# Performance work log

Measured on AMD Instinct MI355X. Metric: run time of the kernel, lower is better.

## Reference

```python
import jax, jax.numpy as jnp
import numpy as np
import math

N0, E, D_IN, H, NC, UH = 4096, 65536, 128, 256, 10, 64
K1 = math.ceil(0.8 * N0)   # 3277 nodes kept by pool1
K2 = math.ceil(0.2 * K1)   # 656 nodes kept by pool2

PARAM_SHAPES = dict(
    gcn1_w=(D_IN, H), gcn1_b=(H,), pool1_w=(H,), gcn2_w=(H, H), gcn2_b=(H,), pool2_w=(H,),
    inr_w=(H, H), inr_b=(H,), ini_w=(H, H), ini_b=(H,),
    enc1_w=(1, UH), enc1_b=(UH,), enc2_w=(UH, UH), enc2_b=(UH,),
    p1_w=(UH, UH), p1_b=(UH,), p2_w=(UH, UH // 2), p2_b=(UH // 2,),
    p3_w=(UH // 2, K2 * K2), p3_b=(K2 * K2,),
    rt_w=(H, H), rt_b=(H,), it_w=(H, H), it_b=(H,),
    msg_wr=(H, H), msg_wi=(H, H),
    mc1_w=(H, H // 2), mc1_b=(H // 2,), mc2_w=(H // 2, NC), mc2_b=(NC,),
    pc1_w=(H, H // 2), pc1_b=(H // 2,), pc2_w=(H // 2, NC), pc2_b=(NC,),
)

def gcn_conv(x, src, dst, emask, W, b):
    # GCNConv: self-loops + symmetric normalization; emask zeroes edges dropped by pooling
    n = x.shape[0]
    h = x @ W
    deg = jnp.zeros((n,), h.dtype).at[dst].add(emask) + 1.0
    dis = jax.lax.rsqrt(deg)
    coef = dis[src] * dis[dst] * emask
    out = jnp.zeros_like(h).at[dst].add(coef[:, None] * h[src])
    out = out + (dis * dis)[:, None] * h   # self-loop contribution
    return out + b

def topk_pool(x, src, dst, emask, w, k):
    # PyG TopKPooling: score = x@w/||w||, keep top-k, x <- x[perm]*tanh(score[perm])
    n = x.shape[0]
    score = (x @ w) / jnp.linalg.norm(w)
    _, perm = jax.lax.top_k(score, k)
    x_new = x[perm] * jnp.tanh(score[perm])[:, None]
    mapping = jnp.full((n,), -1, jnp.int32).at[perm].set(jnp.arange(k, dtype=jnp.int32))
    ns, nd = mapping[src], mapping[dst]
    nm = emask * (ns >= 0) * (nd >= 0)
    return x_new, jnp.maximum(ns, 0), jnp.maximum(nd, 0), nm

def herm_sqrt(C):
    C = (C + C.conj().T) * 0.5
    w, V = jnp.linalg.eigh(C)
    w = jnp.maximum(w, 0.0)
    return (V * jnp.sqrt(w + 1e-8)) @ V.conj().T

def forward(x, edge_index, P):
    src, dst = edge_index[0], edge_index[1]
    em = jnp.ones((src.shape[0],), jnp.float32)
    h = jax.nn.relu(gcn_conv(x, src, dst, em, P['gcn1_w'], P['gcn1_b']))
    h, src, dst, em = topk_pool(h, src, dst, em, P['pool1_w'], K1)
    h = jax.nn.relu(gcn_conv(h, src, dst, em, P['gcn2_w'], P['gcn2_b']))
    h, src, dst, em = topk_pool(h, src, dst, em, P['pool2_w'], K2)
    xr = h @ P['inr_w'] + P['inr_b']
    xi = h @ P['ini_w'] + P['ini_b']
    # --- LocalQuantumLayer (eval mode: dropout is identity) ---
    # ImprovedUnitaryDilationNetwork on the pooled graph (N = K2)
    xg = jnp.ones((K2, 1), jnp.float32)
    xg = jax.nn.relu(gcn_conv(xg, src, dst, em, P['enc1_w'], P['enc1_b']))
    xg = gcn_conv(xg, src, dst, em, P['enc2_w'], P['enc2_b'])
    emb = xg.mean(0)                                     # global_mean_pool, single graph
    t = jax.nn.relu(emb @ P['p1_w'] + P['p1_b'])
    t = jax.nn.relu(t @ P['p2_w'] + P['p2_b'])
    pm = jnp.tanh(t @ P['p3_w'] + P['p3_b']).reshape(K2, K2)
    A = 0.05 * ((pm - pm.T) * 0.5 + 1j * (pm + pm.T) * 0.5)  # antihermitian, scaled
    U = jax.scipy.linalg.expm(A)
    I = jnp.eye(K2, dtype=U.dtype)
    S1 = jax.lax.stop_gradient(herm_sqrt(I - U.conj().T @ U))
    S2 = jax.lax.stop_gradient(herm_sqrt(I - U @ U.conj().T))
    U_dil = jnp.concatenate([jnp.concatenate([U, S1], 1),
                             jnp.concatenate([S2, -U.conj().T], 1)], 0)
    xrt = jax.nn.relu(xr @ P['rt_w'] + P['rt_b'])
    xit = jax.nn.relu(xi @ P['it_w'] + P['it_b'])
    xc = xrt + 1j * xit
    # unitary_dim = 2*K2 > K2 nodes -> single batch, U_sub = U_dil[:K2,:K2]
    evolved = U_dil[:K2, :K2] @ xc
    Wm = P['msg_wr'] + 1j * P['msg_wi']
    msg = evolved[src] @ Wm                              # message(x_j) = x_j @ W (complex)
    agg = jnp.zeros_like(xc).at[dst].add(msg * em[:, None])  # aggr='add'
    outc = agg + (xr + 1j * xi)                          # identity residual (dims equal)
    mag = jnp.abs(outc)
    ph = jnp.arctan2(outc.imag, outc.real)
    gm, gp = mag.mean(0), ph.mean(0)                     # global_mean_pool, single graph
    lm = jax.nn.relu(gm @ P['mc1_w'] + P['mc1_b']) @ P['mc2_w'] + P['mc2_b']
    lp = jax.nn.relu(gp @ P['pc1_w'] + P['pc1_b']) @ P['pc2_w'] + P['pc2_b']
    return lm + lp

def setup_inputs() -> dict:
    key = jax.random.key(0)
    ks = iter(jax.random.split(key, 64))
    inp = {}
    inp['x'] = jax.random.normal(next(ks), (N0, D_IN), jnp.float32)
    inp['edge_index'] = jax.random.randint(next(ks), (2, E), 0, N0)
    for name, shp in PARAM_SHAPES.items():
        inp[name] = jax.random.normal(next(ks), shp, jnp.float32) * 0.05
    return inp

def reference(x, edge_index, gcn1_w, gcn1_b, pool1_w, gcn2_w, gcn2_b, pool2_w, inr_w, inr_b, ini_w, ini_b, enc1_w, enc1_b, enc2_w, enc2_b, p1_w, p1_b, p2_w, p2_b, p3_w, p3_b, rt_w, rt_b, it_w, it_b, msg_wr, msg_wi, mc1_w, mc1_b, mc2_w, mc2_b, pc1_w, pc1_b, pc2_w, pc2_b):
    P = dict(locals())
    x_ = P.pop('x'); ei = P.pop('edge_index')
    return forward(x_, ei, P)
```

## Files before the change

### kernel.cpp

```cpp
#include <hip/hip_runtime.h>
#include <cstddef>
#include <utility>

constexpr int N0  = 4096;
constexpr int E   = 65536;
constexpr int DIN = 128;
constexpr int HD  = 256;
constexpr int NC  = 10;
constexpr int UHD = 64;
constexpr int K1  = 3277;
constexpr int K2  = 656;
constexpr int PMN = K2 * K2;

constexpr int SQ_SLOTS = 4;

constexpr int PLD = 704;
constexpr size_t PPS = (size_t)PLD * PLD;

constexpr int CSPLIT = 8;

#define F4(n) ((size_t)(n) * 4)
constexpr size_t O_H1    = 0;
constexpr size_t O_OUT1  = O_H1    + F4(N0 * HD);
constexpr size_t O_DEG1  = O_OUT1  + F4(N0 * HD);
constexpr size_t O_DIS1  = O_DEG1  + F4(N0);
constexpr size_t O_SC1   = O_DIS1  + F4(N0);
constexpr size_t O_PERM1 = O_SC1   + F4(N0);
constexpr size_t O_MAP1  = O_PERM1 + F4(N0);
constexpr size_t O_H1P   = O_MAP1  + F4(N0);
constexpr size_t O_SRC2  = O_H1P   + F4(K1 * HD);
constexpr size_t O_DST2  = O_SRC2  + F4(E);
constexpr size_t O_EM2   = O_DST2  + F4(E);
constexpr size_t O_H2    = O_EM2   + F4(E);
constexpr size_t O_OUT2  = O_H2    + F4(K1 * HD);
constexpr size_t O_DEG2  = O_OUT2  + F4(K1 * HD);
constexpr size_t O_DIS2  = O_DEG2  + F4(N0);
constexpr size_t O_SC2   = O_DIS2  + F4(N0);
constexpr size_t O_PERM2 = O_SC2   + F4(N0);
constexpr size_t O_MAP2  = O_PERM2 + F4(N0);
constexpr size_t O_H2P   = O_MAP2  + F4(N0);
constexpr size_t O_SRC3  = O_H2P   + F4(K2 * HD);
constexpr size_t O_DST3  = O_SRC3  + F4(E);
constexpr size_t O_EM3   = O_DST3  + F4(E);
constexpr size_t O_XR    = O_EM3   + F4(E);
constexpr size_t O_XI    = O_XR    + F4(K2 * HD);
constexpr size_t O_DEG3  = O_XI    + F4(K2 * HD);
constexpr size_t O_DIS3  = O_DEG3  + F4(1024);
constexpr size_t O_SCOEF = O_DIS3  + F4(1024);
constexpr size_t O_XG1   = O_SCOEF + F4(1024);
constexpr size_t O_XG2H  = O_XG1   + F4(K2 * UHD);
constexpr size_t O_XG2   = O_XG2H  + F4(K2 * UHD);
constexpr size_t O_EMB   = O_XG2   + F4(K2 * UHD);
constexpr size_t O_T1    = O_EMB   + F4(64);
constexpr size_t O_T2    = O_T1    + F4(64);
constexpr size_t O_NORM  = O_T2    + F4(64);
constexpr size_t O_PM    = O_NORM  + F4(64);
constexpr size_t O_BM    = O_PM    + F4(PMN);
constexpr size_t O_P0    = O_BM    + F4(PMN) * 2;
constexpr size_t O_P1    = O_P0    + F4(PMN) * 2;
constexpr size_t O_XRT   = O_P1    + F4(PMN) * 2;
constexpr size_t O_XIT   = O_XRT   + F4(K2 * HD);
constexpr size_t O_XC    = O_XIT   + F4(K2 * HD);
constexpr size_t O_EVO   = O_XC    + F4(K2 * HD) * 2;
constexpr size_t O_AGG0  = O_EVO   + F4(K2 * HD) * 2;
constexpr size_t O_WC    = O_AGG0  + F4(K2 * HD) * 2;
constexpr size_t O_AGG1  = O_WC    + F4(HD * HD) * 2;
constexpr size_t O_MAG   = O_AGG1  + F4(K2 * HD) * 2;
constexpr size_t O_PH    = O_MAG   + F4(K2 * HD);
constexpr size_t O_GM    = O_PH    + F4(K2 * HD);
constexpr size_t O_GP    = O_GM    + F4(256);
constexpr size_t O_HM    = O_GP    + F4(256);
constexpr size_t O_HP    = O_HM    + F4(256);
constexpr size_t O_LM    = O_HP    + F4(256);
constexpr size_t O_LP    = O_LM    + F4(64);
constexpr size_t WS_NEED = O_LP    + F4(64);

constexpr size_t O_SA = 0;
constexpr size_t O_ST = O_SA + PPS * 2 * 4;
static_assert(O_ST + PPS * 2 * 4 <= O_SRC3, "SA/ST must fit in dead region");

constexpr size_t O_B2 = O_XRT;
static_assert(O_B2 + F4(PMN) * 2 <= O_MAG, "B2 must fit in XRT..AGG1 region");

constexpr size_t O_CSR_OFF = O_MAG;
constexpr size_t O_CSR_CUR = O_CSR_OFF + F4(4104);
constexpr size_t O_CSR_SRC = O_CSR_CUR + F4(4104);
constexpr size_t O_CSR_CF  = O_CSR_SRC + F4(E);
static_assert(O_CSR_CF + F4(E) <= O_GM, "CSR must fit in MAG/PH region");

constexpr size_t O_PARTX  = (WS_NEED + 255) & ~(size_t)255;
constexpr size_t PART_SZ  = (size_t)CSPLIT * PMN * 8;
constexpr size_t WS_TOTAL = O_PARTX + PART_SZ;

typedef __attribute__((ext_vector_type(8))) short s8v;
typedef __attribute__((ext_vector_type(4))) float f4v;

__device__ inline unsigned short f2bf(float x) {
  unsigned u = __float_as_uint(x);
  u += 0x7FFFu + ((u >> 16) & 1u);
  return (unsigned short)(u >> 16);
}
__device__ inline float bf2f(unsigned short h) {
  return __uint_as_float(((unsigned)h) << 16);
}
__device__ inline void split4(float re, float im, unsigned short* out,
                              size_t ps, size_t o) {
  unsigned short rh = f2bf(re);
  unsigned short rl = f2bf(re - bf2f(rh));
  unsigned short ih = f2bf(im);
  unsigned short il = f2bf(im - bf2f(ih));
  out[o] = rh; out[ps + o] = rl; out[2 * ps + o] = ih; out[3 * ps + o] = il;
}


template <int ACT>
__global__ void rmm64(const float* __restrict__ A, const float* __restrict__ B,
                      const float* __restrict__ bias, float* __restrict__ C,
                      int M, int N, int K, int CS, int CO) {
  __shared__ float As[64][17];
  __shared__ float Bs[16][64];
  int t  = threadIdx.x;
  int tx = t & 15, ty = t >> 4;
  int bm = blockIdx.y * 64, bn = blockIdx.x * 64;
  float ra[4], rb[4];
#pragma unroll
  for (int i = 0; i < 4; i++) {
    int l = t + i * 256;
    int gr = bm + (l >> 4);
    ra[i] = (gr < M) ? A[(size_t)gr * K + (l & 15)] : 0.f;
    int gc = bn + (l & 63);
    rb[i] = (gc < N) ? B[(size_t)(l >> 6) * N + gc] : 0.f;
  }
  float acc[4][4] = {};
  for (int kt = 0; kt < K; kt += 16) {
#pragma unroll
    for (int i = 0; i < 4; i++) {
      int l = t + i * 256;
      As[l >> 4][l & 15] = ra[i];
      Bs[l >> 6][l & 63] = rb[i];
    }
    __syncthreads();
    int kn = kt + 16;
    if (kn < K) {
#pragma unroll
      for (int i = 0; i < 4; i++) {
// ... 95 lines not shown
  for (int i = 0; i < 4; i++) {
    int r = bm + ty + 16 * i;
    if (r >= M) continue;
#pragma unroll
    for (int j = 0; j < 4; j++) {
      int c = bn + tx + 16 * j;
      if (c >= N) continue;
      float v = acc[i][j] + (bias ? bias[c] : 0.f);
      if (ACT == 1) v = fmaxf(v, 0.f);
      C[((size_t)r * N + c) * CS] = v;
    }
  }
}

__global__ void split_planesT(const float2* __restrict__ in, int inM, int inN,
                              unsigned short* __restrict__ out, int padR, int ld,
                              size_t ps) {
  __shared__ float2 tile[32][33];
  int tx = threadIdx.x & 31, ty = threadIdx.x >> 5;
  int k0 = blockIdx.x * 32, n0 = blockIdx.y * 32;
  for (int i = ty; i < 32; i += 8) {
    int k = k0 + i, n = n0 + tx;
    tile[i][tx] = (k < inM && n < inN) ? in[(size_t)k * inN + n]
                                       : make_float2(0.f, 0.f);
  }
  __syncthreads();
  for (int i = ty; i < 32; i += 8) {
    int n = n0 + i, k = k0 + tx;
    if (n < padR && k < ld)
      split4(tile[tx][i].x, tile[tx][i].y, out, ps, (size_t)n * ld + k);
  }
}

__global__ void split_planesT2(const float* __restrict__ re, const float* __restrict__ im,
                               int inM, int inN, unsigned short* __restrict__ out,
                               int padR, int ld, size_t ps) {
  __shared__ float2 tile[32][33];
  int tx = threadIdx.x & 31, ty = threadIdx.x >> 5;
  int k0 = blockIdx.x * 32, n0 = blockIdx.y * 32;
  for (int i = ty; i < 32; i += 8) {
    int k = k0 + i, n = n0 + tx;
    tile[i][tx] = (k < inM && n < inN)
        ? make_float2(re[(size_t)k * inN + n], im[(size_t)k * inN + n])
        : make_float2(0.f, 0.f);
  }
  __syncthreads();
  for (int i = ty; i < 32; i += 8) {
    int n = n0 + i, k = k0 + tx;
    if (n < padR && k < ld)
      split4(tile[tx][i].x, tile[tx][i].y, out, ps, (size_t)n * ld + k);
  }
}

__global__ __launch_bounds__(256, 2) void cmm_bf16_sk(
    const unsigned short* __restrict__ SA, size_t psA, int ldA,
    const unsigned short* __restrict__ ST, size_t psT, int ldT,
    float2* __restrict__ Part, int M, int N, int Kp, int chunk,
    const int* __restrict__ gate, int slot) {
  if (gate && slot >= *gate - 1) return;
  __shared__ unsigned short Bl[2][4 * 64 * 32];
  int k0 = blockIdx.x * chunk;
  int kend = min(Kp, k0 + chunk);
  int t = threadIdx.x;
  int wave = t >> 6, lane = t & 63;
  int quad = lane >> 4, mn = lane & 15;
  int rowA = blockIdx.z * 64 + wave * 16 + mn;
  int bn = blockIdx.y * 64;
  const unsigned short* a0 = SA + (size_t)rowA * ldA;
  int pB = t >> 6, cB_ = t & 63;
  const unsigned short* bsrc = ST + (size_t)(bn + cB_) * ldT + pB * psT;
  f4v accR[4], accI[4];
#pragma unroll
  for (int i = 0; i < 4; i++) {
    accR[i] = (f4v){0.f, 0.f, 0.f, 0.f};
    accI[i] = (f4v){0.f, 0.f, 0.f, 0.f};
  }
  s8v cA[4], nA[4], rB[4], nB[4];
  {
    int ka = k0 + quad * 8;
#pragma unroll
    for (int p = 0; p < 4; p++) cA[p] = *(const s8v*)(a0 + p * psA + ka);
#pragma unroll
    for (int j = 0; j < 4; j++) rB[j] = *(const s8v*)(bsrc + k0 + j * 8);
  }
  int it = 0;
  for (int kt = k0; kt < kend; kt += 32, ++it) {
    int buf = it & 1;
    unsigned short* bl = &Bl[buf][(size_t)t * 32];
#pragma unroll
    for (int j = 0; j < 4; j++) *(s8v*)(bl + j * 8) = rB[j];
    __syncthreads();
    int kn = kt + 32;
    if (kn < kend) {
      int ka = kn + quad * 8;
#pragma unroll
      for (int p = 0; p < 4; p++) nA[p] = *(const s8v*)(a0 + p * psA + ka);
#pragma unroll
      for (int j = 0; j < 4; j++) nB[j] = *(const s8v*)(bsrc + kn + j * 8);
    }
    s8v nih, nil_;
#pragma unroll
    for (int q = 0; q < 8; q++) {
      nih[q]  = (short)(cA[2][q] ^ (short)0x8000);
      nil_[q] = (short)(cA[3][q] ^ (short)0x8000);
    }
#pragma unroll
    for (int tl = 0; tl < 4; tl++) {
      int c = tl * 16 + mn;
      s8v b0 = *(const s8v*)&Bl[buf][(0 * 64 + c) * 32 + quad * 8];
      s8v b1 = *(const s8v*)&Bl[buf][(1 * 64 + c) * 32 + quad * 8];
      s8v b2 = *(const s8v*)&Bl[buf][(2 * 64 + c) * 32 + quad * 8];
      s8v b3 = *(const s8v*)&Bl[buf][(3 * 64 + c) * 32 + quad * 8];
      f4v r = accR[tl];
      r = __builtin_amdgcn_mfma_f32_16x16x32_bf16(cA[0], b0, r, 0, 0, 0);
      r = __builtin_amdgcn_mfma_f32_16x16x32_bf16(cA[1], b0, r, 0, 0, 0);
      r = __builtin_amdgcn_mfma_f32_16x16x32_bf16(cA[0], b1, r, 0, 0, 0);
      r = __builtin_amdgcn_mfma_f32_16x16x32_bf16(nih, b2, r, 0, 0, 0);
      r = __builtin_amdgcn_mfma_f32_16x16x32_bf16(nil_, b2, r, 0, 0, 0);
      r = __builtin_amdgcn_mfma_f32_16x16x32_bf16(nih, b3, r, 0, 0, 0);
      accR[tl] = r;
      f4v im = accI[tl];
      im = __builtin_amdgcn_mfma_f32_16x16x32_bf16(cA[0], b2, im, 0, 0, 0);
      im = __builtin_amdgcn_mfma_f32_16x16x32_bf16(cA[1], b2, im, 0, 0, 0);
      im = __builtin_amdgcn_mfma_f32_16x16x32_bf16(cA[0], b3, im, 0, 0, 0);
      im = __builtin_amdgcn_mfma_f32_16x16x32_bf16(cA[2], b0, im, 0, 0, 0);
      im = __builtin_amdgcn_mfma_f32_16x16x32_bf16(cA[3], b0, im, 0, 0, 0);
      im = __builtin_amdgcn_mfma_f32_16x16x32_bf16(cA[2], b1, im, 0, 0, 0);
      accI[tl] = im;
    }
    if (kn < kend) {
#pragma unroll
      for (int p = 0; p < 4; p++) cA[p] = nA[p];
#pragma unroll
      for (int j = 0; j < 4; j++) rB[j] = nB[j];
    }
  }
  float2* P = Part + (size_t)blockIdx.x * M * N;
#pragma unroll
  for (int tl = 0; tl < 4; tl++) {
    int col = bn + tl * 16 + mn;
    if (col >= N) continue;
#pragma unroll
    for (int r = 0; r < 4; r++) {
      int row = blockIdx.z * 64 + wave * 16 + quad * 4 + r;
      if (row >= M) continue;
      P[(size_t)row * N + col] = make_float2(accR[tl][r], accI[tl][r]);
    }
  }
}

__global__ void creduce(const float2* __restrict__ Part, float2* __restrict__ C,
                        int MN, int N, int S, float e0,
                        const float2* __restrict__ E1, float e1,
                        const float2* __restrict__ E2, float e2) {
  int idx = blockIdx.x * 256 + threadIdx.x;
  if (idx >= MN) return;
  float sr = 0.f, si = 0.f;
  for (int z = 0; z < S; z++) {
    float2 p = Part[(size_t)z * MN + idx];
    sr += p.x;
    si += p.y;
  }
  if (e0 != 0.f) {
    int r = idx / N;
    if (idx - r * N == r) sr += e0;
  }
  if (E1) { float2 b = E1[idx]; sr += e1 * b.x; si += e1 * b.y; }
  if (E2) { float2 b = E2[idx]; sr += e2 * b.x; si += e2 * b.y; }
  C[idx] = make_float2(sr, si);
}

template <int WC_, int WSA, int WST>
__global__ void creduce_tiled(const float2* __restrict__ Part, int S, int M, int N,
                              int RP, int CP, float2* __restrict__ C,
                              unsigned short* __restrict__ SAp, size_t psA,
                              unsigned short* __restrict__ STp, size_t psT,
                              float e0, const float2* __restrict__ E1, float e1,
                              const float2* __restrict__ E2, float e2,
                              const int* __restrict__ gate, int slot) {
  if (gate && slot >= *gate - 1) return;
  __shared__ float vr[32][33], vi[32][33];
  int tx = threadIdx.x & 31, ty = threadIdx.x >> 5;
  int r0 = blockIdx.y * 32, c0 = blockIdx.x * 32;
  size_t MN = (size_t)M * N;
  for (int i = ty; i < 32; i += 8) {
    int r = r0 + i, c = c0 + tx;
    float sr = 0.f, si = 0.f;
    if (r < M && c < N) {
      size_t o = (size_t)r * N + c;
      for (int z = 0; z < S; z++) {
        float2 p = Part[z * MN + o];
        sr += p.x;
        si += p.y;
      }
      if (e0 != 0.f && r == c) sr += e0;
      if (E1) { float2 b = E1[o]; sr += e1 * b.x; si += e1 * b.y; }
      if (E2) { float2 b = E2[o]; sr += e2 * b.x; si += e2 * b.y; }
      if (WC_) C[o] = make_float2(sr, si);
    }
    if (WSA) split4(sr, si, SAp, psA, (size_t)r * CP + c);
    if (WST) { vr[i][tx] = sr; vi[i][tx] = si; }
  }
  if (WST) {
    __syncthreads();
    for (int i = ty; i < 32; i += 8) {
      int c = c0 + i, r = r0 + tx;
      split4(vr[tx][i], vi[tx][i], STp, psT, (size_t)c * RP + r);
    }
  }
}

__global__ void build_B_split(const float* __restrict__ pm, int n,
                              const float* __restrict__ scale_p,
                              float2* __restrict__ BM,
                              unsigned short* __restrict__ SAp,
                              unsigned short* __restrict__ STp, size_t ps,
                              int RP, int CP) {
  __shared__ float vr[32][33], vi[32][33];
  float scale = scale_p[0];
  int tx = threadIdx.x & 31, ty = threadIdx.x >> 5;
  int r0 = blockIdx.y * 32, c0 = blockIdx.x * 32;
  for (int i = ty; i < 32; i += 8) {
    int r = r0 + i, c = c0 + tx;
    float sr = 0.f, si = 0.f;
    if (r < n && c < n) {
      float pij = pm[(size_t)r * n + c];
      float pji = pm[(size_t)c * n + r];
      sr = scale * (pij - pji);
      si = scale * (pij + pji);
      BM[(size_t)r * n + c] = make_float2(sr, si);
    }
    split4(sr, si, SAp, ps, (size_t)r * CP + c);
    vr[i][tx] = sr;
    vi[i][tx] = si;
  }
  __syncthreads();
  for (int i = ty; i < 32; i += 8) {
    int c = c0 + i, r = r0 + tx;
    split4(vr[tx][i], vi[tx][i], STp, ps, (size_t)c * RP + r);
  }
}

__global__ void anorm_rows(const float* __restrict__ pm, int n,
                           int* __restrict__ anrm, int* __restrict__ done,
                           int* __restrict__ sdev, float* __restrict__ scale) {
  int i = blockIdx.x;
  __shared__ float red[256];
  float s = 0.f;
  for (int j = threadIdx.x; j < n; j += 256) {
    float pij = pm[(size_t)i * n + j];
    float pji = pm[(size_t)j * n + i];
    float a = pij - pji, b = pij + pji;
    s += sqrtf(a * a + b * b);
  }
  red[threadIdx.x] = s;
  __syncthreads();
  for (int off = 128; off > 0; off >>= 1) {
    if (threadIdx.x < off) red[threadIdx.x] += red[threadIdx.x + off];
    __syncthreads();
  }
  if (threadIdx.x == 0) {
    atomicMax(anrm, __float_as_int(red[0] * 0.025f));
    __threadfence();
    int d = atomicAdd(done, 1);
    if (d == gridDim.x - 1) {
      float a = __int_as_float(atomicMax(anrm, 0));
      int sq = (int)ceilf(log2f(fmaxf(a, 1e-20f) / 1.4f));
      sq = min(max(sq, 1), SQ_SLOTS + 1);
      *sdev = sq;
      *scale = 0.025f * exp2f(-(float)sq);
    }
// ... 180 lines not shown
      }
      __syncthreads();
    }
  }
  for (int i = t; i < 4096; i += 1024) {
    int idx = (int)(~(unsigned)(keys[i] & 0xFFFFFFFFull));
    if (idx >= 0) map[idx] = (i < k) ? i : -1;
    if (i < k) perm[i] = idx;
  }
  for (int i = t; i < ncnt; i += 1024) cntz[i] = 0;
}

__global__ void pool_remap(const float* __restrict__ X, const int* __restrict__ perm,
                           const float* __restrict__ dot, const float* __restrict__ normbuf,
                           float* __restrict__ Xn, int F, int k,
                           const int* __restrict__ srcIn, const int* __restrict__ dstIn,
                           const float* __restrict__ emIn, const int* __restrict__ map,
                           int* __restrict__ srcOut, int* __restrict__ dstOut,
                           float* __restrict__ emOut, int* __restrict__ cnt) {
  int b = blockIdx.x;
  if (b < k) {
    int p = perm[b];
    float sc = tanhf(dot[p] / normbuf[0]);
    for (int f = threadIdx.x; f < F; f += blockDim.x)
      Xn[(size_t)b * F + f] = X[(size_t)p * F + f] * sc;
  } else {
    int e = (b - k) * 256 + threadIdx.x;
    if (e >= E) return;
    int ns = map[srcIn[e]], nd = map[dstIn[e]];
    float m = emIn ? emIn[e] : 1.0f;
    if (ns < 0 || nd < 0) m = 0.f;
    srcOut[e] = ns < 0 ? 0 : ns;
    dstOut[e] = nd < 0 ? 0 : nd;
    emOut[e] = m;
    if (m != 0.f) atomicAdd(&cnt[nd], 1);
  }
}

__global__ void col_mean(const float* __restrict__ X, float* __restrict__ out,
                         int rows, int cols) {
  int c = blockIdx.x;
  __shared__ float red[256];
  float s = 0.f;
  for (int r = threadIdx.x; r < rows; r += 256) s += X[(size_t)r * cols + c];
  red[threadIdx.x] = s;
  __syncthreads();
  for (int off = 128; off > 0; off >>= 1) {
    if (threadIdx.x < off) red[threadIdx.x] += red[threadIdx.x + off];
    __syncthreads();
  }
  if (threadIdx.x == 0) out[c] = red[0] / (float)rows;
}

__global__ void magph_mean_part(const float2* __restrict__ Part, int S,
                                const float* __restrict__ xr,
                                const float* __restrict__ xi,
                                float* __restrict__ gm, float* __restrict__ gp,
                                int rows, int cols) {
  int c = blockIdx.x;
  __shared__ float rm[256], rp[256];
  size_t MN = (size_t)rows * cols;
  float sm = 0.f, sp = 0.f;
  for (int r = threadIdx.x; r < rows; r += 256) {
    size_t o = (size_t)r * cols + c;
    float re = xr[o], im = xi[o];
    for (int z = 0; z < S; z++) {
      float2 p = Part[z * MN + o];
      re += p.x;
      im += p.y;
    }
    sm += sqrtf(re * re + im * im);
    sp += atan2f(im, re);
  }
  rm[threadIdx.x] = sm;
  rp[threadIdx.x] = sp;
  __syncthreads();
  for (int off = 128; off > 0; off >>= 1) {
    if (threadIdx.x < off) {
      rm[threadIdx.x] += rm[threadIdx.x + off];
      rp[threadIdx.x] += rp[threadIdx.x + off];
    }
    __syncthreads();
  }
  if (threadIdx.x == 0) {
    gm[c] = rm[0] / (float)rows;
    gp[c] = rp[0] / (float)rows;
  }
}

__global__ void vecmat2(const float* __restrict__ v,
                        const float* __restrict__ W1, const float* __restrict__ b1,
                        const float* __restrict__ W2, const float* __restrict__ b2,
                        float* __restrict__ T2out) {
  __shared__ float vs[64], t1[64];
  int t = threadIdx.x;
  if (t < 64) vs[t] = v[t];
  __syncthreads();
  if (t < 64) {
    float acc = b1[t];
    for (int k = 0; k < 64; k++) acc += vs[k] * W1[(size_t)k * 64 + t];
    t1[t] = fmaxf(acc, 0.f);
  }
  __syncthreads();
  if (t < 32) {
    float acc = b2[t];
    for (int k = 0; k < 64; k++) acc += t1[k] * W2[(size_t)k * 32 + t];
    T2out[t] = fmaxf(acc, 0.f);
  }
}

__global__ void vecmat_tanh_wide(const float* __restrict__ v, const float* __restrict__ W,
                                 const float* __restrict__ b, float* __restrict__ out,
                                 int Kdim, int Ndim, int* __restrict__ anrm_init,
                                 int* __restrict__ done_init) {
  __shared__ float vs[64];
  if (threadIdx.x < Kdim) vs[threadIdx.x] = v[threadIdx.x];
  if (blockIdx.x == 0 && threadIdx.x == 0) { *anrm_init = 0; *done_init = 0; }
  __syncthreads();
  int j = blockIdx.x * 256 + threadIdx.x;
  if (j >= Ndim) return;
// ... 73 lines not shown
  const float* msg_wi  = (const float*)d_in[27];
  const float* mc1_w   = (const float*)d_in[28];
  const float* mc1_b   = (const float*)d_in[29];
  const float* mc2_w   = (const float*)d_in[30];
  const float* mc2_b   = (const float*)d_in[31];
  const float* pc1_w   = (const float*)d_in[32];
  const float* pc1_b   = (const float*)d_in[33];
  const float* pc2_w   = (const float*)d_in[34];
  const float* pc2_b   = (const float*)d_in[35];

  char* ws = (char*)d_ws;
  float*  H1    = (float*)(ws + O_H1);
  float*  OUT1  = (float*)(ws + O_OUT1);
  int*    CNT1  = (int*)(ws + O_DEG1);
  float*  DIS1  = (float*)(ws + O_DIS1);
  float*  SC1   = (float*)(ws + O_SC1);
  int*    PERM1 = (int*)(ws + O_PERM1);
  int*    MAP1  = (int*)(ws + O_MAP1);
  float*  H1P   = (float*)(ws + O_H1P);
  int*    SRC2  = (int*)(ws + O_SRC2);
  int*    DST2  = (int*)(ws + O_DST2);
  float*  EM2   = (float*)(ws + O_EM2);
  float*  H2    = (float*)(ws + O_H2);
  float*  OUT2  = (float*)(ws + O_OUT2);
  int*    CNT2  = (int*)(ws + O_DEG2);
  float*  DIS2  = (float*)(ws + O_DIS2);
  float*  SC2   = (float*)(ws + O_SC2);
  int*    PERM2 = (int*)(ws + O_PERM2);
  int*    MAP2  = (int*)(ws + O_MAP2);
  float*  H2P   = (float*)(ws + O_H2P);
  int*    SRC3  = (int*)(ws + O_SRC3);
  int*    DST3  = (int*)(ws + O_DST3);
  float*  EM3   = (float*)(ws + O_EM3);
  float*  XRb   = (float*)(ws + O_XR);
  float*  XIb   = (float*)(ws + O_XI);
  int*    CNT3  = (int*)(ws + O_DEG3);
  float*  DIS3  = (float*)(ws + O_DIS3);
  float*  XG1   = (float*)(ws + O_XG1);
  float*  XG2H  = (float*)(ws + O_XG2H);
  float*  XG2   = (float*)(ws + O_XG2);
  float*  EMB   = (float*)(ws + O_EMB);
  float*  T2    = (float*)(ws + O_T2);
  float*  NORM  = (float*)(ws + O_NORM);
  int*    ANRM  = (int*)(NORM + 2);
  int*    SDEV  = (int*)(NORM + 3);
  float*  SCALE = NORM + 4;
  int*    DONE  = (int*)(NORM + 5);
  float*  PMV   = (float*)(ws + O_PM);
  float2* BM    = (float2*)(ws + O_BM);
  float2* XC    = (float2*)(ws + O_XC);
  float2* EVO   = (float2*)(ws + O_EVO);
  float*  GM    = (float*)(ws + O_GM);
  float*  GP    = (float*)(ws + O_GP);
  unsigned short* SA = (unsigned short*)(ws + O_SA);
  unsigned short* ST = (unsigned short*)(ws + O_ST);
  float2* PART  = (float2*)(ws + O_PARTX);
  float2* B2v   = (float2*)(ws + O_B2);
  int*    COFF  = (int*)(ws + O_CSR_OFF);
  int*    CCUR  = (int*)(ws + O_CSR_CUR);
  int*    CSRC  = (int*)(ws + O_CSR_SRC);
  float*  CCOEF = (float*)(ws + O_CSR_CF);

  const int* SRC1 = ei;
  const int* DST1 = ei + E;
  const int eg = E / 256;

  rmm64<0><<<dim3(HD / 64, N0 / 64), 256, 0, stream>>>(x, gcn1_w, nullptr, H1, N0, HD, DIN, 1, 0);
  hipMemsetAsync(CNT1, 0, F4(N0), stream);
  hist_edges<<<eg, 256, 0, stream>>>(DST1, nullptr, CNT1);
  scan_offsets<<<1, 1024, 0, stream>>>(CNT1, N0, COFF, CCUR, DIS1);
  fill_edges<<<eg, 256, 0, stream>>>(SRC1, DST1, nullptr, DIS1, CCUR, CSRC, CCOEF);
  gcn_gather<1, 1><<<N0 + 1, 256, 0, stream>>>(COFF, CSRC, CCOEF, H1, DIS1, gcn1_b,
                                               OUT1, HD, N0, pool1_w, SC1, NORM);

  bitonic_topk<<<1, 1024, 0, stream>>>(SC1, N0, PERM1, K1, MAP1, CNT2, K1);
  pool_remap<<<K1 + eg, 256, 0, stream>>>(OUT1, PERM1, SC1, NORM, H1P, HD, K1,
                                          SRC1, DST1, nullptr, MAP1, SRC2, DST2, EM2, CNT2);

  rmm64<0><<<dim3(HD / 64, (K1 + 63) / 64), 256, 0, stream>>>(H1P, gcn2_w, nullptr, H2, K1, HD, HD, 1, 0);
  scan_offsets<<<1, 1024, 0, stream>>>(CNT2, K1, COFF, CCUR, DIS2);
  fill_edges<<<eg, 256, 0, stream>>>(SRC2, DST2, EM2, DIS2, CCUR, CSRC, CCOEF);
  gcn_gather<1, 1><<<K1 + 1, 256, 0, stream>>>(COFF, CSRC, CCOEF, H2, DIS2, gcn2_b,
                                               OUT2, HD, K1, pool2_w, SC2, NORM + 1);

  bitonic_topk<<<1, 1024, 0, stream>>>(SC2, K1, PERM2, K2, MAP2, CNT3, K2);
  pool_remap<<<K2 + eg, 256, 0, stream>>>(OUT2, PERM2, SC2, NORM + 1, H2P, HD, K2,
                                          SRC2, DST2, EM2, MAP2, SRC3, DST3, EM3, CNT3);

  rmm64_dual<0><<<dim3(HD / 64, (K2 + 63) / 64, 2), 256, 0, stream>>>(
      H2P, H2P, inr_w, ini_w, inr_b, ini_b, XRb, XIb, K2, HD, HD, 1);

  scan_offsets<<<1, 1024, 0, stream>>>(CNT3, K2, COFF, CCUR, DIS3);
  fill_edges<<<eg, 256, 0, stream>>>(SRC3, DST3, EM3, DIS3, CCUR, CSRC, CCOEF);

  enc1_fused<<<K2, 64, 0, stream>>>(COFF, CCOEF, DIS3, enc1_w, enc1_b, XG1);
  rmm64<0><<<dim3(UHD / 64, (K2 + 63) / 64), 256, 0, stream>>>(XG1, enc2_w, nullptr, XG2H, K2, UHD, UHD, 1, 0);
  gcn_gather<0, 0><<<K2, 64, 0, stream>>>(COFF, CSRC, CCOEF, XG2H, DIS3, enc2_b,
                                          XG2, UHD, K2, nullptr, nullptr, nullptr);
  col_mean<<<UHD, 256, 0, stream>>>(XG2, EMB, K2, UHD);

  vecmat2<<<1, 64, 0, stream>>>(EMB, p1_w, p1_b, p2_w, p2_b, T2);
  vecmat_tanh_wide<<<(PMN + 255) / 256, 256, 0, stream>>>(T2, p3_w, p3_b, PMV, UHD / 2, PMN, ANRM, DONE);
  anorm_rows<<<K2, 256, 0, stream>>>(PMV, K2, ANRM, DONE, SDEV, SCALE);

  const int sgrid = (PLD * PLD + 255) / 256;
  const dim3 tg22(PLD / 32, PLD / 32);
  const int chF = sk_chunk32(PLD, CSPLIT);
  const dim3 gBig(CSPLIT, 11, 11);
  const float c3 = 1.f / 6.f, c4 = 1.f / 24.f, c5 = 1.f / 120.f;
  const float c6 = 1.f / 720.f, c7 = 1.f / 5040.f, c8 = 1.f / 40320.f;
  const float c9 = 1.f / 362880.f, c10 = 1.f / 3628800.f, c11 = 1.f / 39916800.f;

  build_B_split<<<tg22, 256, 0, stream>>>(PMV, K2, SCALE, BM, SA, ST, PPS, PLD, PLD);
  cmm_bf16_sk<<<gBig, 256, 0, stream>>>(SA, PPS, PLD, ST, PPS, PLD, PART, K2, K2, PLD, chF, nullptr, 0);
  creduce_tiled<1, 1, 0><<<tg22, 256, 0, stream>>>(PART, CSPLIT, K2, K2, PLD, PLD,
      B2v, SA, PPS, nullptr, 0, 0.f, nullptr, 0.f, nullptr, 0.f, nullptr, 0);
  cmm_bf16_sk<<<gBig, 256, 0, stream>>>(SA, PPS, PLD, ST, PPS, PLD, PART, K2, K2, PLD, chF, nullptr, 0);
  creduce_tiled<0, 0, 1><<<tg22, 256, 0, stream>>>(PART, CSPLIT, K2, K2, PLD, PLD,
      nullptr, nullptr, 0, ST, PPS, 0.f, nullptr, 0.f, nullptr, 0.f, nullptr, 0);
  combo3_planes<<<sgrid, 256, 0, stream>>>(BM, B2v, SA, PPS, K2, K2, PLD, PLD, c9, c10, c11);
  cmm_bf16_sk<<<gBig, 256, 0, stream>>>(SA, PPS, PLD, ST, PPS, PLD, PART, K2, K2, PLD, chF, nullptr, 0);
  creduce_tiled<0, 1, 0><<<tg22, 256, 0, stream>>>(PART, CSPLIT, K2, K2, PLD, PLD,
      nullptr, SA, PPS, nullptr, 0, c6, BM, c7, B2v, c8, nullptr, 0);
  cmm_bf16_sk<<<gBig, 256, 0, stream>>>(SA, PPS, PLD, ST, PPS, PLD, PART, K2, K2, PLD, chF, nullptr, 0);
  creduce_tiled<0, 1, 0><<<tg22, 256, 0, stream>>>(PART, CSPLIT, K2, K2, PLD, PLD,
      nullptr, SA, PPS, nullptr, 0, c3, BM, c4, B2v, c5, nullptr, 0);
  cmm_bf16_sk<<<gBig, 256, 0, stream>>>(SA, PPS, PLD, ST, PPS, PLD, PART, K2, K2, PLD, chF, nullptr, 0);
  creduce_tiled<0, 1, 1><<<tg22, 256, 0, stream>>>(PART, CSPLIT, K2, K2, PLD, PLD,
      nullptr, SA, PPS, ST, PPS, 1.f, BM, 1.f, B2v, 0.5f, nullptr, 0);
  for (int t = 0; t < SQ_SLOTS; ++t) {
    cmm_bf16_sk<<<gBig, 256, 0, stream>>>(SA, PPS, PLD, ST, PPS, PLD, PART, K2, K2, PLD, chF, SDEV, t);
    creduce_tiled<0, 1, 1><<<tg22, 256, 0, stream>>>(PART, CSPLIT, K2, K2, PLD, PLD,
        nullptr, SA, PPS, ST, PPS, 0.f, nullptr, 0.f, nullptr, 0.f, SDEV, t);
  }

  rmm64_dual<1><<<dim3(HD / 64, (K2 + 63) / 64, 2), 256, 0, stream>>>(
      XRb, XIb, rt_w, it_w, rt_b, it_b, (float*)XC, (float*)XC + 1, K2, HD, HD, 2);
  {
    const int mn = K2 * HD;
    const int rg = (mn + 255) / 256;
    const dim3 gSkin(CSPLIT, HD / 64, 11);
    const size_t psX = (size_t)HD * PLD;
    split_planesT<<<dim3((PLD + 31) / 32, (HD + 31) / 32), 256, 0, stream>>>(
        XC, K2, HD, ST, HD, PLD, psX);
    cmm_bf16_sk<<<gSkin, 256, 0, stream>>>(SA, PPS, PLD, ST, psX, PLD, PART, K2, HD, PLD, chF, nullptr, 0);
    creduce_tiled<0, 0, 1><<<dim3(HD / 32, PLD / 32), 256, 0, stream>>>(
        PART, CSPLIT, K2, HD, PLD, HD, nullptr, nullptr, 0, ST, psX,
        0.f, nullptr, 0.f, nullptr, 0.f, nullptr, 0);
    cmm_bf16_sk<<<gSkin, 256, 0, stream>>>(SA, PPS, PLD, ST, psX, PLD, PART, K2, HD, PLD, chF, nullptr, 0);
    creduce<<<rg, 256, 0, stream>>>(PART, EVO, mn, HD, CSPLIT, 0.f, nullptr, 0.f, nullptr, 0.f);
    const size_t psG = (size_t)PLD * HD;
    agg_gather_split<<<PLD, 256, 0, stream>>>(COFF, CSRC, EVO, SA, psG, HD, K2);
    split_planesT2<<<dim3((HD + 31) / 32, (HD + 31) / 32), 256, 0, stream>>>(
        msg_wr, msg_wi, HD, HD, ST, HD, HD, (size_t)HD * HD);
    cmm_bf16_sk<<<gSkin, 256, 0, stream>>>(SA, psG, HD, ST, (size_t)HD * HD, HD, PART,
                                           K2, HD, HD, sk_chunk32(HD, CSPLIT), nullptr, 0);
    magph_mean_part<<<HD, 256, 0, stream>>>(PART, CSPLIT, XRb, XIb, GM, GP, K2, HD);
  }

  heads_fused<<<1, 256, 0, stream>>>(GM, GP, mc1_w, mc1_b, mc2_w, mc2_b,
                                     pc1_w, pc1_b, pc2_w, pc2_b, (float*)d_out);
}
```

Measured before the change: 731.3 us.

## Fuse split-K reduction into complex GEMM via last-block tile counters

Merges the separate creduce/creduce_tiled passes into the complex bf16 split-K GEMM. Each output tile has an atomic counter, and the last-arriving K-slice block sums the partials and applies the epilogue (identity/E1/E2 terms, split into bf16 planes, transposed output). Ping-pong SA/ST buffers are added, and gated squaring slots copy the planes forward, which removes about a dozen kernel launches and their extra passes over the partial buffer. In exchange, one block per tile does a serial reduction over its slices, the code needs fences, atomics and counter resets, and the workspace grows.

```diff
diff --git a/kernel.cpp b/kernel.cpp
--- a/kernel.cpp
+++ b/kernel.cpp
@@ -16,6 +16,8 @@
 
 constexpr int PLD = 704;
 constexpr size_t PPS = (size_t)PLD * PLD;
+constexpr size_t PSX = (size_t)HD * PLD;
+constexpr size_t PSW = (size_t)HD * HD;
 
 constexpr int CSPLIT = 8;
 
@@ -89,8 +91,15 @@
 static_assert(O_CSR_CF + F4(E) <= O_GM, "CSR must fit in MAG/PH region");
 
 constexpr size_t O_PARTX  = (WS_NEED + 255) & ~(size_t)255;
-constexpr size_t PART_SZ  = (size_t)CSPLIT * PMN * 8;
-constexpr size_t WS_TOTAL = O_PARTX + PART_SZ;
+constexpr size_t PART_SZ  = (size_t)CSPLIT * PPS * 8;
+constexpr size_t O_SA1    = O_PARTX + ((PART_SZ + 255) & ~(size_t)255);
+constexpr size_t O_ST1    = O_SA1 + PPS * 2 * 4;
+constexpr size_t O_XCTP   = O_ST1 + PPS * 2 * 4;
+constexpr size_t O_TTP    = O_XCTP + PSX * 2 * 4;
+constexpr size_t O_AGGP   = O_TTP + PSX * 2 * 4;
+constexpr size_t O_WTP    = O_AGGP + PSX * 2 * 4;
+constexpr size_t O_TCNT   = O_WTP + PSW * 2 * 4;
+constexpr size_t WS_TOTAL = O_TCNT + F4(128);
 
 typedef __attribute__((ext_vector_type(8))) short s8v;
 typedef __attribute__((ext_vector_type(4))) float f4v;
@@ -292,20 +301,43 @@
   }
 }
 
-__global__ __launch_bounds__(256, 2) void cmm_bf16_sk(
+__global__ __launch_bounds__(256, 2) void cmm_fix(
     const unsigned short* __restrict__ SA, size_t psA, int ldA,
     const unsigned short* __restrict__ ST, size_t psT, int ldT,
     float2* __restrict__ Part, int M, int N, int Kp, int chunk,
-    const int* __restrict__ gate, int slot) {
-  if (gate && slot >= *gate - 1) return;
+    const int* __restrict__ gate, int slot,
+    int* __restrict__ tcnt,
+    float2* __restrict__ Cout, int Cn,
+    unsigned short* __restrict__ oSA, size_t opsA,
+    unsigned short* __restrict__ oST, size_t opsT, int oRP,
+    float e0, const float2* __restrict__ E1, float e1,
+    const float2* __restrict__ E2, float e2,
+    const unsigned short* __restrict__ cpSA, const unsigned short* __restrict__ cpST) {
+  int t = threadIdx.x;
+  int Np = gridDim.y << 6;
+  if (gate && slot >= *gate - 1) {
+    if (blockIdx.x != 0 || !cpSA) return;
+    int r0 = blockIdx.z << 6, c0 = blockIdx.y << 6;
+    for (int p = 0; p < 4; p++) {
+      for (int idx = t; idx < 4096; idx += 256) {
+        int r = r0 + (idx >> 6), c = c0 + (idx & 63);
+        oSA[p * opsA + (size_t)r * Np + c] = cpSA[p * psA + (size_t)r * ldA + c];
+      }
+      for (int idx = t; idx < 4096; idx += 256) {
+        int c = c0 + (idx >> 6), r = r0 + (idx & 63);
+        oST[p * opsT + (size_t)c * oRP + r] = cpST[p * psT + (size_t)c * oRP + r];
+      }
+    }
+    return;
+  }
   __shared__ unsigned short Bl[2][4 * 64 * 32];
+  __shared__ int es;
   int k0 = blockIdx.x * chunk;
   int kend = min(Kp, k0 + chunk);
-  int t = threadIdx.x;
   int wave = t >> 6, lane = t & 63;
   int quad = lane >> 4, mn = lane & 15;
-  int rowA = blockIdx.z * 64 + wave * 16 + mn;
-  int bn = blockIdx.y * 64;
+  int rowA = (blockIdx.z << 6) + wave * 16 + mn;
+  int bn = blockIdx.y << 6;
   const unsigned short* a0 = SA + (size_t)rowA * ldA;
   int pB = t >> 6, cB_ = t & 63;
   const unsigned short* bsrc = ST + (size_t)(bn + cB_) * ldT + pB * psT;
@@ -375,77 +407,51 @@
       for (int j = 0; j < 4; j++) rB[j] = nB[j];
     }
   }
-  float2* P = Part + (size_t)blockIdx.x * M * N;
+  size_t MpNp = (size_t)(gridDim.z << 6) * Np;
+  float2* P = Part + (size_t)blockIdx.x * MpNp;
 #pragma unroll
   for (int tl = 0; tl < 4; tl++) {
     int col = bn + tl * 16 + mn;
-    if (col >= N) continue;
 #pragma unroll
     for (int r = 0; r < 4; r++) {
-      int row = blockIdx.z * 64 + wave * 16 + quad * 4 + r;
-      if (row >= M) continue;
-      P[(size_t)row * N + col] = make_float2(accR[tl][r], accI[tl][r]);
-    }
-  }
-}
-
-__global__ void creduce(const float2* __restrict__ Part, float2* __restrict__ C,
-                        int MN, int N, int S, float e0,
-                        const float2* __restrict__ E1, float e1,
-                        const float2* __restrict__ E2, float e2) {
-  int idx = blockIdx.x * 256 + threadIdx.x;
-  if (idx >= MN) return;
-  float sr = 0.f, si = 0.f;
-  for (int z = 0; z < S; z++) {
-    float2 p = Part[(size_t)z * MN + idx];
-    sr += p.x;
-    si += p.y;
-  }
-  if (e0 != 0.f) {
-    int r = idx / N;
-    if (idx - r * N == r) sr += e0;
-  }
-  if (E1) { float2 b = E1[idx]; sr += e1 * b.x; si += e1 * b.y; }
-  if (E2) { float2 b = E2[idx]; sr += e2 * b.x; si += e2 * b.y; }
-  C[idx] = make_float2(sr, si);
-}
-
-template <int WC_, int WSA, int WST>
-__global__ void creduce_tiled(const float2* __restrict__ Part, int S, int M, int N,
-                              int RP, int CP, float2* __restrict__ C,
-                              unsigned short* __restrict__ SAp, size_t psA,
-                              unsigned short* __restrict__ STp, size_t psT,
-                              float e0, const float2* __restrict__ E1, float e1,
-                              const float2* __restrict__ E2, float e2,
-                              const int* __restrict__ gate, int slot) {
-  if (gate && slot >= *gate - 1) return;
-  __shared__ float vr[32][33], vi[32][33];
-  int tx = threadIdx.x & 31, ty = threadIdx.x >> 5;
-  int r0 = blockIdx.y * 32, c0 = blockIdx.x * 32;
-  size_t MN = (size_t)M * N;
-  for (int i = ty; i < 32; i += 8) {
-    int r = r0 + i, c = c0 + tx;
-    float sr = 0.f, si = 0.f;
-    if (r < M && c < N) {
-      size_t o = (size_t)r * N + c;
-      for (int z = 0; z < S; z++) {
-        float2 p = Part[z * MN + o];
+      int row = (blockIdx.z << 6) + wave * 16 + quad * 4 + r;
+      P[(size_t)row * Np + col] = make_float2(accR[tl][r], accI[tl][r]);
+    }
+  }
+  if (!tcnt) return;
+  __threadfence();
+  if (t == 0) {
+    int ti = blockIdx.z * gridDim.y + blockIdx.y;
+    int d = atomicAdd(&tcnt[ti], 1);
+    es = (d == (int)gridDim.x - 1);
+    if (es) tcnt[ti] = 0;
+  }
+  __syncthreads();
+  if (!es) return;
+  __threadfence();
+  int Z = gridDim.x;
+#pragma unroll
+  for (int tl = 0; tl < 4; tl++) {
+    int col = bn + tl * 16 + mn;
+#pragma unroll
+    for (int r = 0; r < 4; r++) {
+      int row = (blockIdx.z << 6) + wave * 16 + quad * 4 + r;
+      size_t po = (size_t)row * Np + col;
+      float sr = 0.f, si = 0.f;
+      for (int z = 0; z < Z; z++) {
+        float2 p = Part[(size_t)z * MpNp + po];
         sr += p.x;
         si += p.y;
       }
-      if (e0 != 0.f && r == c) sr += e0;
-      if (E1) { float2 b = E1[o]; sr += e1 * b.x; si += e1 * b.y; }
-      if (E2) { float2 b = E2[o]; sr += e2 * b.x; si += e2 * b.y; }
-      if (WC_) C[o] = make_float2(sr, si);
-    }
-    if (WSA) split4(sr, si, SAp, psA, (size_t)r * CP + c);
-    if (WST) { vr[i][tx] = sr; vi[i][tx] = si; }
-  }
-  if (WST) {
-    __syncthreads();
-    for (int i = ty; i < 32; i += 8) {
-      int c = c0 + i, r = r0 + tx;
-      split4(vr[tx][i], vi[tx][i], STp, psT, (size_t)c * RP + r);
+      if (row < M && col < N) {
+        if (e0 != 0.f && row == col) sr += e0;
+        size_t eo = (size_t)row * N + col;
+        if (E1) { float2 b = E1[eo]; sr += e1 * b.x; si += e1 * b.y; }
+        if (E2) { float2 b = E2[eo]; sr += e2 * b.x; si += e2 * b.y; }
+        if (Cout) Cout[(size_t)row * Cn + col] = make_float2(sr, si);
+      }
+      if (oSA) split4(sr, si, oSA, opsA, (size_t)row * Np + col);
+      if (oST) split4(sr, si, oST, opsT, (size_t)col * oRP + row);
     }
   }
 }
@@ -455,8 +461,10 @@
                               float2* __restrict__ BM,
                               unsigned short* __restrict__ SAp,
                               unsigned short* __restrict__ STp, size_t ps,
-                              int RP, int CP) {
+                              int RP, int CP, int* __restrict__ tcnt) {
   __shared__ float vr[32][33], vi[32][33];
+  if (blockIdx.x == 0 && blockIdx.y == 0 && threadIdx.x < 128)
+    tcnt[threadIdx.x] = 0;
   float scale = scale_p[0];
   int tx = threadIdx.x & 31, ty = threadIdx.x >> 5;
   int r0 = blockIdx.y * 32, c0 = blockIdx.x * 32;
@@ -743,20 +751,19 @@
   if (threadIdx.x == 0) out[c] = red[0] / (float)rows;
 }
 
-__global__ void magph_mean_part(const float2* __restrict__ Part, int S,
+__global__ void magph_mean_part(const float2* __restrict__ Part, int S, size_t slc,
                                 const float* __restrict__ xr,
                                 const float* __restrict__ xi,
                                 float* __restrict__ gm, float* __restrict__ gp,
                                 int rows, int cols) {
   int c = blockIdx.x;
   __shared__ float rm[256], rp[256];
-  size_t MN = (size_t)rows * cols;
   float sm = 0.f, sp = 0.f;
   for (int r = threadIdx.x; r < rows; r += 256) {
     size_t o = (size_t)r * cols + c;
     float re = xr[o], im = xi[o];
     for (int z = 0; z < S; z++) {
-      float2 p = Part[z * MN + o];
+      float2 p = Part[z * slc + o];
       re += p.x;
       im += p.y;
     }
@@ -936,8 +943,15 @@
   float2* EVO   = (float2*)(ws + O_EVO);
   float*  GM    = (float*)(ws + O_GM);
   float*  GP    = (float*)(ws + O_GP);
-  unsigned short* SA = (unsigned short*)(ws + O_SA);
-  unsigned short* ST = (unsigned short*)(ws + O_ST);
+  unsigned short* SA0 = (unsigned short*)(ws + O_SA);
+  unsigned short* ST0 = (unsigned short*)(ws + O_ST);
+  unsigned short* SA1 = (unsigned short*)(ws + O_SA1);
+  unsigned short* ST1 = (unsigned short*)(ws + O_ST1);
+  unsigned short* XCTP = (unsigned short*)(ws + O_XCTP);
+  unsigned short* TTP  = (unsigned short*)(ws + O_TTP);
+  unsigned short* AGGP = (unsigned short*)(ws + O_AGGP);
+  unsigned short* WTP  = (unsigned short*)(ws + O_WTP);
+  int*    TCNT  = (int*)(ws + O_TCNT);
   float2* PART  = (float2*)(ws + O_PARTX);
   float2* B2v   = (float2*)(ws + O_B2);
   int*    COFF  = (int*)(ws + O_CSR_OFF);
@@ -995,51 +1009,51 @@
   const float c6 = 1.f / 720.f, c7 = 1.f / 5040.f, c8 = 1.f / 40320.f;
   const float c9 = 1.f / 362880.f, c10 = 1.f / 3628800.f, c11 = 1.f / 39916800.f;
 
-  build_B_split<<<tg22, 256, 0, stream>>>(PMV, K2, SCALE, BM, SA, ST, PPS, PLD, PLD);
-  cmm_bf16_sk<<<gBig, 256, 0, stream>>>(SA, PPS, PLD, ST, PPS, PLD, PART, K2, K2, PLD, chF, nullptr, 0);
-  creduce_tiled<1, 1, 0><<<tg22, 256, 0, stream>>>(PART, CSPLIT, K2, K2, PLD, PLD,
-      B2v, SA, PPS, nullptr, 0, 0.f, nullptr, 0.f, nullptr, 0.f, nullptr, 0);
-  cmm_bf16_sk<<<gBig, 256, 0, stream>>>(SA, PPS, PLD, ST, PPS, PLD, PART, K2, K2, PLD, chF, nullptr, 0);
-  creduce_tiled<0, 0, 1><<<tg22, 256, 0, stream>>>(PART, CSPLIT, K2, K2, PLD, PLD,
-      nullptr, nullptr, 0, ST, PPS, 0.f, nullptr, 0.f, nullptr, 0.f, nullptr, 0);
-  combo3_planes<<<sgrid, 256, 0, stream>>>(BM, B2v, SA, PPS, K2, K2, PLD, PLD, c9, c10, c11);
-  cmm_bf16_sk<<<gBig, 256, 0, stream>>>(SA, PPS, PLD, ST, PPS, PLD, PART, K2, K2, PLD, chF, nullptr, 0);
-  creduce_tiled<0, 1, 0><<<tg22, 256, 0, stream>>>(PART, CSPLIT, K2, K2, PLD, PLD,
-      nullptr, SA, PPS, nullptr, 0, c6, BM, c7, B2v, c8, nullptr, 0);
-  cmm_bf16_sk<<<gBig, 256, 0, stream>>>(SA, PPS, PLD, ST, PPS, PLD, PART, K2, K2, PLD, chF, nullptr, 0);
-  creduce_tiled<0, 1, 0><<<tg22, 256, 0, stream>>>(PART, CSPLIT, K2, K2, PLD, PLD,
-      nullptr, SA, PPS, nullptr, 0, c3, BM, c4, B2v, c5, nullptr, 0);
-  cmm_bf16_sk<<<gBig, 256, 0, stream>>>(SA, PPS, PLD, ST, PPS, PLD, PART, K2, K2, PLD, chF, nullptr, 0);
-  creduce_tiled<0, 1, 1><<<tg22, 256, 0, stream>>>(PART, CSPLIT, K2, K2, PLD, PLD,
-      nullptr, SA, PPS, ST, PPS, 1.f, BM, 1.f, B2v, 0.5f, nullptr, 0);
+  build_B_split<<<tg22, 256, 0, stream>>>(PMV, K2, SCALE, BM, SA0, ST0, PPS, PLD, PLD, TCNT);
+  cmm_fix<<<gBig, 256, 0, stream>>>(SA0, PPS, PLD, ST0, PPS, PLD, PART, K2, K2, PLD, chF,
+      nullptr, 0, TCNT, B2v, K2, SA1, PPS, nullptr, 0, 0,
+      0.f, nullptr, 0.f, nullptr, 0.f, nullptr, nullptr);
+  cmm_fix<<<gBig, 256, 0, stream>>>(SA1, PPS, PLD, ST0, PPS, PLD, PART, K2, K2, PLD, chF,
+      nullptr, 0, TCNT, nullptr, 0, nullptr, 0, ST1, PPS, PLD,
+      0.f, nullptr, 0.f, nullptr, 0.f, nullptr, nullptr);
+  combo3_planes<<<sgrid, 256, 0, stream>>>(BM, B2v, SA0, PPS, K2, K2, PLD, PLD, c9, c10, c11);
+  cmm_fix<<<gBig, 256, 0, stream>>>(SA0, PPS, PLD, ST1, PPS, PLD, PART, K2, K2, PLD, chF,
+      nullptr, 0, TCNT, nullptr, 0, SA1, PPS, nullptr, 0, 0,
+      c6, BM, c7, B2v, c8, nullptr, nullptr);
+  cmm_fix<<<gBig, 256, 0, stream>>>(SA1, PPS, PLD, ST1, PPS, PLD, PART, K2, K2, PLD, chF,
+      nullptr, 0, TCNT, nullptr, 0, SA0, PPS, nullptr, 0, 0,
+      c3, BM, c4, B2v, c5, nullptr, nullptr);
+  cmm_fix<<<gBig, 256, 0, stream>>>(SA0, PPS, PLD, ST1, PPS, PLD, PART, K2, K2, PLD, chF,
+      nullptr, 0, TCNT, nullptr, 0, SA1, PPS, ST0, PPS, PLD,
+      1.f, BM, 1.f, B2v, 0.5f, nullptr, nullptr);
+  unsigned short* sqa[5] = {SA1, SA0, SA1, SA0, SA1};
+  unsigned short* sqt[5] = {ST0, ST1, ST0, ST1, ST0};
   for (int t = 0; t < SQ_SLOTS; ++t) {
-    cmm_bf16_sk<<<gBig, 256, 0, stream>>>(SA, PPS, PLD, ST, PPS, PLD, PART, K2, K2, PLD, chF, SDEV, t);
-    creduce_tiled<0, 1, 1><<<tg22, 256, 0, stream>>>(PART, CSPLIT, K2, K2, PLD, PLD,
-        nullptr, SA, PPS, ST, PPS, 0.f, nullptr, 0.f, nullptr, 0.f, SDEV, t);
+    cmm_fix<<<gBig, 256, 0, stream>>>(sqa[t], PPS, PLD, sqt[t], PPS, PLD, PART, K2, K2, PLD, chF,
+        SDEV, t, TCNT, nullptr, 0, sqa[t + 1], PPS, sqt[t + 1], PPS, PLD,
+        0.f, nullptr, 0.f, nullptr, 0.f, sqa[t], sqt[t]);
   }
 
   rmm64_dual<1><<<dim3(HD / 64, (K2 + 63) / 64, 2), 256, 0, stream>>>(
       XRb, XIb, rt_w, it_w, rt_b, it_b, (float*)XC, (float*)XC + 1, K2, HD, HD, 2);
   {
-    const int mn = K2 * HD;
-    const int rg = (mn + 255) / 256;
     const dim3 gSkin(CSPLIT, HD / 64, 11);
-    const size_t psX = (size_t)HD * PLD;
     split_planesT<<<dim3((PLD + 31) / 32, (HD + 31) / 32), 256, 0, stream>>>(
-        XC, K2, HD, ST, HD, PLD, psX);
-    cmm_bf16_sk<<<gSkin, 256, 0, stream>>>(SA, PPS, PLD, ST, psX, PLD, PART, K2, HD, PLD, chF, nullptr, 0);
-    creduce_tiled<0, 0, 1><<<dim3(HD / 32, PLD / 32), 256, 0, stream>>>(
-        PART, CSPLIT, K2, HD, PLD, HD, nullptr, nullptr, 0, ST, psX,
-        0.f, nullptr, 0.f, nullptr, 0.f, nullptr, 0);
-    cmm_bf16_sk<<<gSkin, 256, 0, stream>>>(SA, PPS, PLD, ST, psX, PLD, PART, K2, HD, PLD, chF, nullptr, 0);
-    creduce<<<rg, 256, 0, stream>>>(PART, EVO, mn, HD, CSPLIT, 0.f, nullptr, 0.f, nullptr, 0.f);
-    const size_t psG = (size_t)PLD * HD;
-    agg_gather_split<<<PLD, 256, 0, stream>>>(COFF, CSRC, EVO, SA, psG, HD, K2);
+        XC, K2, HD, XCTP, HD, PLD, PSX);
+    cmm_fix<<<gSkin, 256, 0, stream>>>(SA1, PPS, PLD, XCTP, PSX, PLD, PART, K2, HD, PLD, chF,
+        nullptr, 0, TCNT, nullptr, 0, nullptr, 0, TTP, PSX, PLD,
+        0.f, nullptr, 0.f, nullptr, 0.f, nullptr, nullptr);
+    cmm_fix<<<gSkin, 256, 0, stream>>>(SA1, PPS, PLD, TTP, PSX, PLD, PART, K2, HD, PLD, chF,
+        nullptr, 0, TCNT, EVO, HD, nullptr, 0, nullptr, 0, 0,
+        0.f, nullptr, 0.f, nullptr, 0.f, nullptr, nullptr);
+    agg_gather_split<<<PLD, 256, 0, stream>>>(COFF, CSRC, EVO, AGGP, PSX, HD, K2);
     split_planesT2<<<dim3((HD + 31) / 32, (HD + 31) / 32), 256, 0, stream>>>(
-        msg_wr, msg_wi, HD, HD, ST, HD, HD, (size_t)HD * HD);
-    cmm_bf16_sk<<<gSkin, 256, 0, stream>>>(SA, psG, HD, ST, (size_t)HD * HD, HD, PART,
-                                           K2, HD, HD, sk_chunk32(HD, CSPLIT), nullptr, 0);
-    magph_mean_part<<<HD, 256, 0, stream>>>(PART, CSPLIT, XRb, XIb, GM, GP, K2, HD);
+        msg_wr, msg_wi, HD, HD, WTP, HD, HD, PSW);
+    cmm_fix<<<gSkin, 256, 0, stream>>>(AGGP, PSX, HD, WTP, PSW, HD, PART, K2, HD, HD,
+        sk_chunk32(HD, CSPLIT), nullptr, 0, nullptr, nullptr, 0, nullptr, 0, nullptr, 0, 0,
+        0.f, nullptr, 0.f, nullptr, 0.f, nullptr, nullptr);
+    magph_mean_part<<<HD, 256, 0, stream>>>(PART, CSPLIT, (size_t)PLD * HD,
+                                            XRb, XIb, GM, GP, K2, HD);
   }
 
   heads_fused<<<1, 256, 0, stream>>>(GM, GP, mc1_w, mc1_b, mc2_w, mc2_b,
```

Measured after the change: 2.264 ms. +209.6%, slower.
